# Performance work log

Hardware: AMD Instinct MI355X
Metric: run time of the kernel (lower is better)

## Reference

```python
import jax, jax.numpy as jnp
import numpy as np

T, B, DX, DH, DZ, K = 128, 256, 64, 512, 128, 16


def _lin(x, W, b):
    return x @ W.T + b


def _forget_mult(F, Z, h0):
    # C[t] = F[t]*Z[t] + (1-F[t])*C[t-1], C[-1] = h0; shapes (T,B,H)
    def step(c, fz):
        f, z = fz
        c = f * z + (1.0 - f) * c
        return c, c
    _, C = jax.lax.scan(step, h0, (F, Z))
    return C


def _qrnn_layer(X, W, b, h0):
    # window=1, output_gate=True, zoneout=0 (eval)
    Y = _lin(X, W, b)                      # (T,B,3H)
    Z, F, O = jnp.split(Y, 3, axis=-1)
    C = _forget_mult(jax.nn.sigmoid(F), jnp.tanh(Z), h0)
    return jax.nn.sigmoid(O) * C           # H


def _planar_flow(z, u, w, b):
    # z: (B,T,Dz); u,w: (K,Dz); b: (K,). Returns z_K and summed log-det.
    def m(x):
        return jax.nn.softplus(x) - 1.0
    def step(carry, p):
        z, sldj = carry
        uk, wk, bk = p
        udw = jnp.dot(uk, wk)
        w_hat = wk / jnp.linalg.norm(wk)
        u_hat = (m(udw) - udw) * w_hat + uk
        t = jnp.tanh(z @ wk + bk)          # (B,T)
        z = z + u_hat * t[..., None]
        psi_u = (1.0 - t * t) * jnp.dot(wk, u_hat)
        sldj = sldj - jnp.log(jnp.abs(psi_u + 1.0) + 1e-8)
        return (z, sldj), None
    sldj0 = jnp.zeros(z.shape[:-1], z.dtype)
    (zK, sldj), _ = jax.lax.scan(step, (z, sldj0), (u, w, b))
    return zK, sldj


def _forward(x, y, eps, hs_W, hs_b, q_W, q_b, enc_phi_W, enc_phi_b,
             enc_mean_W, enc_mean_b, enc_std_W, enc_std_b,
             prior_phi_W, prior_phi_b, prior_mean_W, prior_mean_b,
             prior_std_W, prior_std_b, dec_phi_W1, dec_phi_b1,
             dec_phi_W2, dec_phi_b2, dec_mean_W, dec_mean_b,
             dec_std_W, dec_std_b, pnf_u, pnf_w, pnf_b):
    Bsz = x.shape[1]
    Dh = hs_W.shape[0] // 3
    h0 = jnp.zeros((Bsz, Dh), x.dtype)
    # hidden-state QRNN over x
    h = _qrnn_layer(x, hs_W, hs_b, h0)                 # (T,B,Dh)
    # inference QRNN over reversed [y, h]
    rev_in = jnp.concatenate([jnp.flip(y, 0), jnp.flip(h, 0)], axis=-1)
    a = _qrnn_layer(rev_in, q_W, q_b, h0)              # (T,B,Dh)
    rev_a = jnp.swapaxes(jnp.flip(a, 0), 0, 1)         # (B,T,Dh)
    # encoder
    e = jax.nn.relu(_lin(rev_a, enc_phi_W[0], enc_phi_b[0]))
    e = jax.nn.relu(_lin(e, enc_phi_W[1], enc_phi_b[1]))
    enc_mean = jax.nn.sigmoid(_lin(e, enc_mean_W, enc_mean_b))   # (B,T,Dz)
    enc_std = jax.nn.softplus(_lin(e, enc_std_W, enc_std_b))
    z0 = enc_mean + enc_std * eps
    z_k, sldj = _planar_flow(z0, pnf_u, pnf_w, pnf_b)
    # prior
    hp = jnp.swapaxes(h, 0, 1)                          # (B,T,Dh)
    p = jax.nn.relu(_lin(hp, prior_phi_W[0], prior_phi_b[0]))
    p = jax.nn.relu(_lin(p, prior_phi_W[1], prior_phi_b[1]))
    prior_mean = jax.nn.sigmoid(_lin(p, prior_mean_W, prior_mean_b))
    prior_std = jax.nn.softplus(_lin(p, prior_std_W, prior_std_b))
    # decoder
    d = jax.nn.relu(_lin(jnp.concatenate([z_k, hp], axis=-1), dec_phi_W1, dec_phi_b1))
    d = jax.nn.relu(_lin(d, dec_phi_W2, dec_phi_b2))
    dec_mean = jax.nn.sigmoid(_lin(d, dec_mean_W, dec_mean_b))   # (B,T,Dx)
    dec_std = jax.nn.softplus(_lin(d, dec_std_W, dec_std_b))
    return dec_mean, dec_std, enc_mean, enc_std, prior_mean, prior_std, z_k, sldj


def setup_inputs() -> dict:
    key = jax.random.key(0)
    ks = jax.random.split(key, 20)
    def w(i, shape, scale=0.05):
        return (jax.random.normal(ks[i], shape) * scale).astype(jnp.float32)
    return {
        "x": w(0, (T, B, DX), 1.0),
        "y": w(1, (T, B, DX), 1.0),
        "eps": w(2, (B, T, DZ), 1.0),
        "hs_W": w(3, (3 * DH, DX)), "hs_b": jnp.zeros((3 * DH,), jnp.float32),
        "q_W": w(4, (3 * DH, DX + DH)), "q_b": jnp.zeros((3 * DH,), jnp.float32),
        "enc_phi_W": w(5, (2, DH, DH)), "enc_phi_b": jnp.zeros((2, DH), jnp.float32),
        "enc_mean_W": w(6, (DZ, DH)), "enc_mean_b": jnp.zeros((DZ,), jnp.float32),
        "enc_std_W": w(7, (DZ, DH)), "enc_std_b": jnp.zeros((DZ,), jnp.float32),
        "prior_phi_W": w(8, (2, DH, DH)), "prior_phi_b": jnp.zeros((2, DH), jnp.float32),
        "prior_mean_W": w(9, (DZ, DH)), "prior_mean_b": jnp.zeros((DZ,), jnp.float32),
        "prior_std_W": w(10, (DZ, DH)), "prior_std_b": jnp.zeros((DZ,), jnp.float32),
        "dec_phi_W1": w(11, (DH, DH + DZ)), "dec_phi_b1": jnp.zeros((DH,), jnp.float32),
        "dec_phi_W2": w(12, (DH, DH)), "dec_phi_b2": jnp.zeros((DH,), jnp.float32),
        "dec_mean_W": w(13, (DX, DH)), "dec_mean_b": jnp.zeros((DX,), jnp.float32),
        "dec_std_W": w(14, (DX, DH)), "dec_std_b": jnp.zeros((DX,), jnp.float32),
        "pnf_u": w(15, (K, DZ), 0.01), "pnf_w": w(16, (K, DZ), 0.01), "pnf_b": w(17, (K,), 0.01),
    }


def reference(x, y, eps, hs_W, hs_b, q_W, q_b, enc_phi_W, enc_phi_b,
              enc_mean_W, enc_mean_b, enc_std_W, enc_std_b,
              prior_phi_W, prior_phi_b, prior_mean_W, prior_mean_b,
              prior_std_W, prior_std_b, dec_phi_W1, dec_phi_b1,
              dec_phi_W2, dec_phi_b2, dec_mean_W, dec_mean_b,
              dec_std_W, dec_std_b, pnf_u, pnf_w, pnf_b):
    return _forward(x, y, eps, hs_W, hs_b, q_W, q_b, enc_phi_W, enc_phi_b,
                    enc_mean_W, enc_mean_b, enc_std_W, enc_std_b,
                    prior_phi_W, prior_phi_b, prior_mean_W, prior_mean_b,
                    prior_std_W, prior_std_b, dec_phi_W1, dec_phi_b1,
                    dec_phi_W2, dec_phi_b2, dec_mean_W, dec_mean_b,
                    dec_std_W, dec_std_b, pnf_u, pnf_w, pnf_b)
```

## Files before the change

kernel.cpp:

```cpp
#include <hip/hip_runtime.h>
#include <cstddef>
#include <cstdint>

#define DEVI __device__ __forceinline__

namespace {

typedef _Float16 f16;
typedef _Float16 half4 __attribute__((ext_vector_type(4)));
typedef _Float16 half8 __attribute__((ext_vector_type(8)));
typedef _Float16 f16x2 __attribute__((ext_vector_type(2)));
typedef float floatx16 __attribute__((ext_vector_type(16)));

typedef const __attribute__((address_space(1))) void gvoid;
typedef __attribute__((address_space(3))) void lvoid;
#define GLL(gp, lp) __builtin_amdgcn_global_load_lds((gvoid*)(gp), (lvoid*)(lp), 16, 0, 0)

constexpr float kLog2e = 1.4426950408889634f;
constexpr float kLn2   = 0.6931471805599453f;
DEVI float fexp2_(float x) { return __builtin_amdgcn_exp2f(x); }
DEVI float frcp_(float x)  { return __builtin_amdgcn_rcpf(x); }
DEVI float flog2_(float x) { return __builtin_amdgcn_logf(x); }
DEVI float fsig_(float v)  { return frcp_(1.f + fexp2_(-kLog2e * v)); }
DEVI float ftanh_(float v) { return 1.f - 2.f * frcp_(1.f + fexp2_(2.f * kLog2e * v)); }
DEVI float fsoftplus_(float v) {
  return fmaxf(v, 0.f) + kLn2 * flog2_(1.f + fexp2_(-kLog2e * fabsf(v)));
}

struct CvtTab { const float* s[14]; f16* d[14]; int n4[14]; };

__global__ __launch_bounds__(256)
void cvt_k(CvtTab tab) {
  const int e = blockIdx.y;
  const int n4 = tab.n4[e];
  const float4* s = (const float4*)tab.s[e];
  f16* d = tab.d[e];
  for (int i = blockIdx.x * 256 + threadIdx.x; i < n4; i += gridDim.x * 256) {
    const float4 v = s[i];
    half4 o = {(f16)v.x, (f16)v.y, (f16)v.z, (f16)v.w};
    *(half4*)(d + (size_t)i * 4) = o;
  }
}

template <int AM, int OM>
__global__ __launch_bounds__(512, 2)
void gemm16_k(const f16* __restrict__ A0, const f16* __restrict__ A1,
              const f16* __restrict__ W0, const f16* __restrict__ W1,
              const float* __restrict__ bias, const float* __restrict__ bias2,
              float* __restrict__ C, float* __restrict__ C2,
              f16* __restrict__ Ch, int N, int K, int lda, int ntx) {
  __shared__ __align__(16) char lds[131072];
  const int tid = threadIdx.x;
  const int l = tid & 63, w = tid >> 6;
  const int nwg = gridDim.x;
  int bid = blockIdx.x;
  bid = (bid & 7) * (nwg >> 3) + (bid >> 3);
  const int m0 = (bid / ntx) * 256;
  const int n0 = (bid % ntx) * 256;
  const int Nh = N >> 1;

  const f16* pa[4]; const f16* pa2[4]; const f16* pb[4];
#pragma unroll
  for (int r = 0; r < 4; ++r) {
    const int s = r * 512 + tid;
    const int row = s >> 3, c = s & 7;
    const int kc8 = (c ^ (row & 7)) * 8;
    const int m = m0 + row;
    if constexpr (AM == 0) {
      pa[r] = A0 + (size_t)m * lda + kc8;
      pa2[r] = nullptr;
    } else if constexpr (AM == 1) {
      const int t = m >> 8, b = m & 255;
      pa[r]  = A0 + (size_t)((127 - t) * 256 + b) * 64 + kc8;
      pa2[r] = A1 + (size_t)((b << 7) | (127 - t)) * 512 + kc8;
    } else {
      pa[r]  = A0 + (size_t)m * 128 + kc8;
      pa2[r] = A1 + (size_t)m * 512 + kc8;
    }
    int n = n0 + row;
    if constexpr (OM == 2) n = n < N ? n : N - 1;
    if constexpr (OM == 2) {
      pb[r] = (n < Nh ? W0 + (size_t)n * K : W1 + (size_t)(n - Nh) * K) + kc8;
    } else {
      pb[r] = W0 + (size_t)n * K + kc8;
    }
  }

  const int wr = w >> 2, wc = w & 3;
  int offA[4][4], offB[2][4];
#pragma unroll
  for (int mi = 0; mi < 4; ++mi) {
    const int row = wr * 128 + mi * 32 + (l & 31);
#pragma unroll
    for (int s16 = 0; s16 < 4; ++s16) {
      const int c = (s16 * 2 + (l >> 5)) ^ (row & 7);
      offA[mi][s16] = row * 128 + c * 16;
    }
  }
#pragma unroll
  for (int nj = 0; nj < 2; ++nj) {
    const int row = wc * 64 + nj * 32 + (l & 31);
#pragma unroll
    for (int s16 = 0; s16 < 4; ++s16) {
      const int c = (s16 * 2 + (l >> 5)) ^ (row & 7);
      offB[nj][s16] = row * 128 + c * 16;
    }
  }

  float bv[2];
#pragma unroll
  for (int nj = 0; nj < 2; ++nj) {
    int gcol = n0 + wc * 64 + nj * 32 + (l & 31);
    if constexpr (OM == 2) {
      const int gi = gcol < N ? gcol : N - 1;
      bv[nj] = (gi >= Nh) ? bias2[gi - Nh] : bias[gi];
    } else {
      bv[nj] = bias[gcol];
    }
  }
  asm volatile("" : "+v"(bv[0]), "+v"(bv[1]));
  asm volatile("s_waitcnt vmcnt(0)" ::: "memory");

  auto stage = [&](int st, int buf) {
    char* dA = lds + buf * 65536;
    char* dB = dA + 32768;
#pragma unroll
    for (int r = 0; r < 4; ++r) {
      const f16* ga;
      if constexpr (AM == 0)      ga = pa[r] + st * 64;
      else if constexpr (AM == 1) ga = (st == 0) ? pa[r] : (pa2[r] + (st - 1) * 64);
      else                        ga = (st < 2) ? (pa[r] + st * 64) : (pa2[r] + (st - 2) * 64);
      GLL(ga, dA + (r * 512 + w * 64) * 16);
      GLL(pb[r] + st * 64, dB + (r * 512 + w * 64) * 16);
    }
  };

  floatx16 acc[4][2] = {};
  const int nsteps = K >> 6;
  stage(0, 0);
  for (int st = 0; st < nsteps; ++st) {
    const int cur = st & 1;
    if (st + 1 < nsteps) {
      stage(st + 1, cur ^ 1);
      asm volatile("s_waitcnt vmcnt(8)" ::: "memory");
    } else {
      asm volatile("s_waitcnt vmcnt(0)" ::: "memory");
    }
    __builtin_amdgcn_s_barrier();
    __builtin_amdgcn_sched_barrier(0);
    const char* cA = lds + cur * 65536;
    const char* cB = cA + 32768;
#pragma unroll
    for (int s16 = 0; s16 < 4; ++s16) {
      half8 a0 = *(const half8*)(cA + offA[0][s16]);
      half8 a1 = *(const half8*)(cA + offA[1][s16]);
      half8 a2 = *(const half8*)(cA + offA[2][s16]);
      half8 a3 = *(const half8*)(cA + offA[3][s16]);
      half8 b0 = *(const half8*)(cB + offB[0][s16]);
      half8 b1 = *(const half8*)(cB + offB[1][s16]);
      acc[0][0] = __builtin_amdgcn_mfma_f32_32x32x16_f16(a0, b0, acc[0][0], 0, 0, 0);
      acc[0][1] = __builtin_amdgcn_mfma_f32_32x32x16_f16(a0, b1, acc[0][1], 0, 0, 0);
      acc[1][0] = __builtin_amdgcn_mfma_f32_32x32x16_f16(a1, b0, acc[1][0], 0, 0, 0);
      acc[1][1] = __builtin_amdgcn_mfma_f32_32x32x16_f16(a1, b1, acc[1][1], 0, 0, 0);
      acc[2][0] = __builtin_amdgcn_mfma_f32_32x32x16_f16(a2, b0, acc[2][0], 0, 0, 0);
      acc[2][1] = __builtin_amdgcn_mfma_f32_32x32x16_f16(a2, b1, acc[2][1], 0, 0, 0);
      acc[3][0] = __builtin_amdgcn_mfma_f32_32x32x16_f16(a3, b0, acc[3][0], 0, 0, 0);
      acc[3][1] = __builtin_amdgcn_mfma_f32_32x32x16_f16(a3, b1, acc[3][1], 0, 0, 0);
    }
    __builtin_amdgcn_sched_barrier(0);
    asm volatile("s_waitcnt lgkmcnt(0)" ::: "memory");
    __builtin_amdgcn_s_barrier();
  }

  const int col_l = l & 31;
  const int hi4 = (l >> 5) * 4;
#pragma unroll
  for (int nj = 0; nj < 2; ++nj) {
    const int gcol = n0 + wc * 64 + nj * 32 + col_l;
    if constexpr (OM == 2) {
      if (gcol < N) {
        const bool second = gcol >= Nh;
        float* cp = second ? C2 : C;
        const int cl = second ? gcol - Nh : gcol;
#pragma unroll
        for (int mi = 0; mi < 4; ++mi) {
#pragma unroll
          for (int reg = 0; reg < 16; ++reg) {
            const int rl = (reg & 3) + 8 * (reg >> 2) + hi4;
            const int grow = m0 + wr * 128 + mi * 32 + rl;
            const float v = acc[mi][nj][reg] + bv[nj];
            cp[(size_t)grow * Nh + cl] = second ? fsoftplus_(v) : fsig_(v);
          }
        }
      }
    } else {
#pragma unroll
      for (int mi = 0; mi < 4; ++mi) {
#pragma unroll
        for (int reg = 0; reg < 16; ++reg) {
          const int rl = (reg & 3) + 8 * (reg >> 2) + hi4;
          const int grow = m0 + wr * 128 + mi * 32 + rl;
          const float v = acc[mi][nj][reg] + bv[nj];
          float rr;
          if constexpr (OM == 0) rr = (gcol < 512) ? ftanh_(v) : fsig_(v);
          else                   rr = fmaxf(v, 0.f);
          Ch[(size_t)grow * N + gcol] = (f16)rr;
        }
      }
    }
  }
}

template <int MODE>
__global__ __launch_bounds__(256)
void scan_k(const f16* __restrict__ Y, f16* __restrict__ H1) {
  const int idx = blockIdx.x * 256 + threadIdx.x;
  const int b = idx >> 8;
  const int h0 = (idx & 255) * 2;
  float c0 = 0.f, c1 = 0.f;
  for (int t = 0; t < 128; ++t) {
    const f16* p = Y + (size_t)(t * 256 + b) * 1536 + h0;
    const f16x2 zv = *(const f16x2*)(p);
    const f16x2 fv = *(const f16x2*)(p + 512);
    const f16x2 ov = *(const f16x2*)(p + 1024);
    const float f0 = (float)fv[0], f1 = (float)fv[1];
    c0 = f0 * (float)zv[0] + (1.f - f0) * c0;
    c1 = f1 * (float)zv[1] + (1.f - f1) * c1;
    f16x2 hv = {(f16)((float)ov[0] * c0), (f16)((float)ov[1] * c1)};
    const int tt = (MODE == 0) ? t : (127 - t);
    *(f16x2*)(H1 + (size_t)((b << 7) | tt) * 512 + h0) = hv;
  }
}

__global__ __launch_bounds__(256)
void z0_k(const float* __restrict__ mean, const float* __restrict__ sd,
          const float* __restrict__ eps, float* __restrict__ z) {
  const int i = blockIdx.x * 256 + threadIdx.x;
  const float4 m = ((const float4*)mean)[i];
  const float4 s = ((const float4*)sd)[i];
  const float4 e = ((const float4*)eps)[i];
  ((float4*)z)[i] = make_float4(m.x + s.x * e.x, m.y + s.y * e.y,
                                m.z + s.z * e.z, m.w + s.w * e.w);
}

__global__ __launch_bounds__(64)
void flow_pre_k(const float* __restrict__ u, const float* __restrict__ w,
                float* __restrict__ uhat, float* __restrict__ wu) {
  const int k = blockIdx.x, l = threadIdx.x;
  const float w0 = w[k * 128 + l], w1 = w[k * 128 + 64 + l];
  const float u0 = u[k * 128 + l], u1 = u[k * 128 + 64 + l];
  float nrm = w0 * w0 + w1 * w1;
  float udw = u0 * w0 + u1 * w1;
#pragma unroll
  for (int o = 32; o; o >>= 1) { nrm += __shfl_xor(nrm, o); udw += __shfl_xor(udw, o); }
  const float inv = 1.f / sqrtf(nrm);
  const float coef = (fsoftplus_(udw) - 1.f) - udw;
  const float uh0 = coef * (w0 * inv) + u0;
  const float uh1 = coef * (w1 * inv) + u1;
  uhat[k * 128 + l] = uh0;
  uhat[k * 128 + 64 + l] = uh1;
  float dwu = w0 * uh0 + w1 * uh1;
#pragma unroll
  for (int o = 32; o; o >>= 1) dwu += __shfl_xor(dwu, o);
  if (l == 0) wu[k] = dwu;
}

__global__ __launch_bounds__(256)
void flow_k(float* __restrict__ z, const float* __restrict__ w,
            const float* __restrict__ b, const float* __restrict__ uhat,
            const float* __restrict__ wu, float* __restrict__ sldj,
            f16* __restrict__ zh) {
  const int row = blockIdx.x * 4 + (threadIdx.x >> 6);
  const int l = threadIdx.x & 63;
  float* zp = z + (size_t)row * 128;
  float z0 = zp[l], z1 = zp[64 + l];
  float sl = 0.f;
#pragma unroll
  for (int k = 0; k < 16; ++k) {
    const float w0 = w[k * 128 + l], w1 = w[k * 128 + 64 + l];
    float s = z0 * w0 + z1 * w1;
#pragma unroll
    for (int o = 32; o; o >>= 1) s += __shfl_xor(s, o);
    const float t = ftanh_(s + b[k]);
    z0 += uhat[k * 128 + l] * t;
    z1 += uhat[k * 128 + 64 + l] * t;
    const float psi = (1.f - t * t) * wu[k];
    sl -= kLn2 * flog2_(fabsf(psi + 1.f) + 1e-8f);
  }
  zp[l] = z0;
  zp[64 + l] = z1;
  zh[(size_t)row * 128 + l] = (f16)z0;
  zh[(size_t)row * 128 + 64 + l] = (f16)z1;
  if (l == 0) sldj[row] = sl;
}

}

extern "C" void kernel_launch(void* const* d_in, const int* in_sizes, int n_in,
                              void* d_out, int out_size, void* d_ws, size_t ws_size,
                              hipStream_t stream) {
  const float* x           = (const float*)d_in[0];
  const float* y           = (const float*)d_in[1];
  const float* eps         = (const float*)d_in[2];
  const float* hs_b        = (const float*)d_in[4];
  const float* q_b         = (const float*)d_in[6];
  const float* enc_phi_b   = (const float*)d_in[8];
  const float* enc_mean_b  = (const float*)d_in[10];
  const float* enc_std_b   = (const float*)d_in[12];
  const float* prior_phi_b = (const float*)d_in[14];
  const float* prior_mean_b= (const float*)d_in[16];
  const float* prior_std_b = (const float*)d_in[18];
  const float* dec_b1      = (const float*)d_in[20];
  const float* dec_b2      = (const float*)d_in[22];
  const float* dec_mean_b  = (const float*)d_in[24];
  const float* dec_std_b   = (const float*)d_in[26];
  const float* pnf_u       = (const float*)d_in[27];
  const float* pnf_w       = (const float*)d_in[28];
  const float* pnf_b       = (const float*)d_in[29];

  float* out = (float*)d_out;
  float* dec_mean  = out;
  float* dec_std   = out + 2097152;
  float* enc_mean  = out + 4194304;
  float* enc_std   = out + 8388608;
  float* prior_mean= out + 12582912;
  float* prior_std = out + 16777216;
  float* zk        = out + 20971520;
  float* sldj      = out + 25165824;

  char* ws = (char*)d_ws;
  f16* Ybuf  = (f16*)(ws + 0);
  f16* e1    = (f16*)(ws + 0);
  f16* e2    = (f16*)(ws + 33554432);
  f16* arev  = (f16*)(ws + 100663296);
  f16* h_bt  = (f16*)(ws + 134217728);
  f16* zk_h  = (f16*)(ws + 167772160);
  f16* xh    = (f16*)(ws + 176160768);
  f16* yh    = (f16*)(ws + 180355072);
  f16* wbuf  = (f16*)(ws + 184549376);
  float* uhat= (float*)(ws + 190447616);
  float* wu  = (float*)(ws + 190455808);

  f16* w_hs   = wbuf + 0;
  f16* w_q    = wbuf + 98304;
  f16* w_ephi = wbuf + 983040;
  f16* w_emean= wbuf + 1507328;
  f16* w_estd = wbuf + 1572864;
  f16* w_pphi = wbuf + 1638400;
  f16* w_pmean= wbuf + 2162688;
  f16* w_pstd = wbuf + 2228224;
  f16* w_d1   = wbuf + 2293760;
  f16* w_d2   = wbuf + 2621440;
  f16* w_dmean= wbuf + 2883584;
  f16* w_dstd = wbuf + 2916352;

  CvtTab tab;
  const float* srcs[14] = {x, y, (const float*)d_in[3], (const float*)d_in[5],
                           (const float*)d_in[7], (const float*)d_in[9],
                           (const float*)d_in[11], (const float*)d_in[13],
                           (const float*)d_in[15], (const float*)d_in[17],
                           (const float*)d_in[19], (const float*)d_in[21],
                           (const float*)d_in[23], (const float*)d_in[25]};
  f16* dsts[14] = {xh, yh, w_hs, w_q, w_ephi, w_emean, w_estd, w_pphi,
                   w_pmean, w_pstd, w_d1, w_d2, w_dmean, w_dstd};
  const int ns[14] = {2097152, 2097152, 98304, 884736, 524288, 65536, 65536,
                      524288, 65536, 65536, 327680, 262144, 32768, 32768};
  for (int i = 0; i < 14; ++i) { tab.s[i] = srcs[i]; tab.d[i] = dsts[i]; tab.n4[i] = ns[i] >> 2; }
  cvt_k<<<dim3(128, 14), 256, 0, stream>>>(tab);

  const dim3 blk(512);

  gemm16_k<0, 0><<<768, blk, 0, stream>>>(xh, nullptr, w_hs, nullptr,
      hs_b, nullptr, nullptr, nullptr, Ybuf, 1536, 64, 64, 6);
  scan_k<0><<<256, 256, 0, stream>>>(Ybuf, h_bt);

  gemm16_k<1, 0><<<768, blk, 0, stream>>>(yh, h_bt, w_q, nullptr,
      q_b, nullptr, nullptr, nullptr, Ybuf, 1536, 576, 0, 6);
  scan_k<1><<<256, 256, 0, stream>>>(Ybuf, arev);

  gemm16_k<0, 1><<<256, blk, 0, stream>>>(arev, nullptr, w_ephi, nullptr,
      enc_phi_b, nullptr, nullptr, nullptr, e1, 512, 512, 512, 2);
  gemm16_k<0, 1><<<256, blk, 0, stream>>>(e1, nullptr, w_ephi + 262144, nullptr,
      enc_phi_b + 512, nullptr, nullptr, nullptr, e2, 512, 512, 512, 2);
  gemm16_k<0, 2><<<128, blk, 0, stream>>>(e2, nullptr, w_emean, w_estd,
      enc_mean_b, enc_std_b, enc_mean, enc_std, nullptr, 256, 512, 512, 1);
  z0_k<<<4096, 256, 0, stream>>>(enc_mean, enc_std, eps, zk);
  flow_pre_k<<<16, 64, 0, stream>>>(pnf_u, pnf_w, uhat, wu);
  flow_k<<<8192, 256, 0, stream>>>(zk, pnf_w, pnf_b, uhat, wu, sldj, zk_h);

  gemm16_k<0, 1><<<256, blk, 0, stream>>>(h_bt, nullptr, w_pphi, nullptr,
      prior_phi_b, nullptr, nullptr, nullptr, e1, 512, 512, 512, 2);
  gemm16_k<0, 1><<<256, blk, 0, stream>>>(e1, nullptr, w_pphi + 262144, nullptr,
      prior_phi_b + 512, nullptr, nullptr, nullptr, e2, 512, 512, 512, 2);
  gemm16_k<0, 2><<<128, blk, 0, stream>>>(e2, nullptr, w_pmean, w_pstd,
      prior_mean_b, prior_std_b, prior_mean, prior_std, nullptr, 256, 512, 512, 1);

  gemm16_k<2, 1><<<256, blk, 0, stream>>>(zk_h, h_bt, w_d1, nullptr,
      dec_b1, nullptr, nullptr, nullptr, e1, 512, 640, 0, 2);
  gemm16_k<0, 1><<<256, blk, 0, stream>>>(e1, nullptr, w_d2, nullptr,
      dec_b2, nullptr, nullptr, nullptr, e2, 512, 512, 512, 2);
  gemm16_k<0, 2><<<128, blk, 0, stream>>>(e2, nullptr, w_dmean, w_dstd,
      dec_mean_b, dec_std_b, dec_mean, dec_std, nullptr, 128, 512, 512, 1);
}
```

Before: 649.3 us.

## Switch GEMM to 16x16 MFMA with interleaved chunked staging; prefetch scan loads

The GEMM main loop now uses 16x16x32 MFMA tiles (8x4 per wave) and splits the next-stage global-to-LDS copy into four chunks interleaved with compute phases. It adds barriers and s_setprio around each MFMA burst so load issue overlaps matrix work, in place of issuing all loads up front. The scan kernel software-prefetches the next timestep's z/f/o values to hide global load latency in the serial recurrence. The extra barriers per step and a full vmcnt(0) wait at the end of each step may cost some of the intended overlap.

```diff
diff --git a/kernel.cpp b/kernel.cpp
--- a/kernel.cpp
+++ b/kernel.cpp
@@ -10,7 +10,7 @@
 typedef _Float16 half4 __attribute__((ext_vector_type(4)));
 typedef _Float16 half8 __attribute__((ext_vector_type(8)));
 typedef _Float16 f16x2 __attribute__((ext_vector_type(2)));
-typedef float floatx16 __attribute__((ext_vector_type(16)));
+typedef float floatx4 __attribute__((ext_vector_type(4)));
 
 typedef const __attribute__((address_space(1))) void gvoid;
 typedef __attribute__((address_space(3))) void lvoid;
@@ -59,7 +59,7 @@
   const int n0 = (bid % ntx) * 256;
   const int Nh = N >> 1;
 
-  const f16* pa[4]; const f16* pa2[4]; const f16* pb[4];
+  const f16 *pa[4], *pa2[4], *pb[4];
 #pragma unroll
   for (int r = 0; r < 4; ++r) {
     const int s = r * 512 + tid;
@@ -87,120 +87,127 @@
   }
 
   const int wr = w >> 2, wc = w & 3;
-  int offA[4][4], offB[2][4];
-#pragma unroll
-  for (int mi = 0; mi < 4; ++mi) {
-    const int row = wr * 128 + mi * 32 + (l & 31);
-#pragma unroll
-    for (int s16 = 0; s16 < 4; ++s16) {
-      const int c = (s16 * 2 + (l >> 5)) ^ (row & 7);
-      offA[mi][s16] = row * 128 + c * 16;
-    }
-  }
-#pragma unroll
-  for (int nj = 0; nj < 2; ++nj) {
-    const int row = wc * 64 + nj * 32 + (l & 31);
-#pragma unroll
-    for (int s16 = 0; s16 < 4; ++s16) {
-      const int c = (s16 * 2 + (l >> 5)) ^ (row & 7);
-      offB[nj][s16] = row * 128 + c * 16;
-    }
-  }
-
-  float bv[2];
-#pragma unroll
-  for (int nj = 0; nj < 2; ++nj) {
-    int gcol = n0 + wc * 64 + nj * 32 + (l & 31);
+  int offA[8][2], offB[4][2];
+#pragma unroll
+  for (int mf = 0; mf < 8; ++mf) {
+    const int row = wr * 128 + mf * 16 + (l & 15);
+#pragma unroll
+    for (int ks = 0; ks < 2; ++ks) {
+      const int c = (ks * 4 + (l >> 4)) ^ (row & 7);
+      offA[mf][ks] = row * 128 + c * 16;
+    }
+  }
+#pragma unroll
+  for (int nf = 0; nf < 4; ++nf) {
+    const int row = wc * 64 + nf * 16 + (l & 15);
+#pragma unroll
+    for (int ks = 0; ks < 2; ++ks) {
+      const int c = (ks * 4 + (l >> 4)) ^ (row & 7);
+      offB[nf][ks] = row * 128 + c * 16;
+    }
+  }
+
+  float bv[4];
+#pragma unroll
+  for (int nf = 0; nf < 4; ++nf) {
+    int gcol = n0 + wc * 64 + nf * 16 + (l & 15);
     if constexpr (OM == 2) {
       const int gi = gcol < N ? gcol : N - 1;
-      bv[nj] = (gi >= Nh) ? bias2[gi - Nh] : bias[gi];
+      bv[nf] = (gi >= Nh) ? bias2[gi - Nh] : bias[gi];
     } else {
-      bv[nj] = bias[gcol];
-    }
-  }
-  asm volatile("" : "+v"(bv[0]), "+v"(bv[1]));
-  asm volatile("s_waitcnt vmcnt(0)" ::: "memory");
-
-  auto stage = [&](int st, int buf) {
+      bv[nf] = bias[gcol];
+    }
+  }
+
+  auto stage_chunk = [&](int st, int buf, int p) {
     char* dA = lds + buf * 65536;
     char* dB = dA + 32768;
 #pragma unroll
-    for (int r = 0; r < 4; ++r) {
-      const f16* ga;
-      if constexpr (AM == 0)      ga = pa[r] + st * 64;
-      else if constexpr (AM == 1) ga = (st == 0) ? pa[r] : (pa2[r] + (st - 1) * 64);
-      else                        ga = (st < 2) ? (pa[r] + st * 64) : (pa2[r] + (st - 2) * 64);
-      GLL(ga, dA + (r * 512 + w * 64) * 16);
-      GLL(pb[r] + st * 64, dB + (r * 512 + w * 64) * 16);
+    for (int q = 0; q < 2; ++q) {
+      const int r = (p & 1) * 2 + q;
+      if (p < 2) {
+        const f16* ga;
+        if constexpr (AM == 0)      ga = pa[r] + st * 64;
+        else if constexpr (AM == 1) ga = (st == 0) ? pa[r] : (pa2[r] + (st - 1) * 64);
+        else                        ga = (st < 2) ? (pa[r] + st * 64) : (pa2[r] + (st - 2) * 64);
+        GLL(ga, dA + (r * 512 + w * 64) * 16);
+      } else {
+        GLL(pb[r] + st * 64, dB + (r * 512 + w * 64) * 16);
+      }
     }
   };
 
-  floatx16 acc[4][2] = {};
+  floatx4 acc[8][4] = {};
   const int nsteps = K >> 6;
-  stage(0, 0);
-  for (int st = 0; st < nsteps; ++st) {
-    const int cur = st & 1;
-    if (st + 1 < nsteps) {
-      stage(st + 1, cur ^ 1);
-      asm volatile("s_waitcnt vmcnt(8)" ::: "memory");
-    } else {
-      asm volatile("s_waitcnt vmcnt(0)" ::: "memory");
-    }
+#pragma unroll
+  for (int p = 0; p < 4; ++p) stage_chunk(0, 0, p);
+  asm volatile("s_waitcnt vmcnt(0)" ::: "memory");
+  __builtin_amdgcn_s_barrier();
+
+  for (int t = 0; t < nsteps; ++t) {
+    const int s = t & 1;
+    const char* cA = lds + s * 65536;
+    const char* cB = cA + 32768;
+    const bool more = (t + 1 < nsteps);
+    half8 bfr[4];
+#pragma unroll
+    for (int p = 0; p < 4; ++p) {
+      if (more) stage_chunk(t + 1, s ^ 1, p);
+      constexpr int dummy = 0; (void)dummy;
+      const int ks = p >> 1;
+      if ((p & 1) == 0) {
+        bfr[0] = *(const half8*)(cB + offB[0][ks]);
+        bfr[1] = *(const half8*)(cB + offB[1][ks]);
+        bfr[2] = *(const half8*)(cB + offB[2][ks]);
+        bfr[3] = *(const half8*)(cB + offB[3][ks]);
+      }
+      half8 afr[4];
+#pragma unroll
+      for (int mi = 0; mi < 4; ++mi)
+        afr[mi] = *(const half8*)(cA + offA[(p & 1) * 4 + mi][ks]);
+      __builtin_amdgcn_s_barrier();
+      __builtin_amdgcn_s_setprio(1);
+#pragma unroll
+      for (int mi = 0; mi < 4; ++mi) {
+#pragma unroll
+        for (int nf = 0; nf < 4; ++nf) {
+          acc[(p & 1) * 4 + mi][nf] = __builtin_amdgcn_mfma_f32_16x16x32_f16(
+              afr[mi], bfr[nf], acc[(p & 1) * 4 + mi][nf], 0, 0, 0);
+        }
+      }
+      __builtin_amdgcn_s_setprio(0);
+      __builtin_amdgcn_s_barrier();
+    }
+    asm volatile("s_waitcnt lgkmcnt(0) vmcnt(0)" ::: "memory");
     __builtin_amdgcn_s_barrier();
-    __builtin_amdgcn_sched_barrier(0);
-    const char* cA = lds + cur * 65536;
-    const char* cB = cA + 32768;
-#pragma unroll
-    for (int s16 = 0; s16 < 4; ++s16) {
-      half8 a0 = *(const half8*)(cA + offA[0][s16]);
-      half8 a1 = *(const half8*)(cA + offA[1][s16]);
-      half8 a2 = *(const half8*)(cA + offA[2][s16]);
-      half8 a3 = *(const half8*)(cA + offA[3][s16]);
-      half8 b0 = *(const half8*)(cB + offB[0][s16]);
-      half8 b1 = *(const half8*)(cB + offB[1][s16]);
-      acc[0][0] = __builtin_amdgcn_mfma_f32_32x32x16_f16(a0, b0, acc[0][0], 0, 0, 0);
-      acc[0][1] = __builtin_amdgcn_mfma_f32_32x32x16_f16(a0, b1, acc[0][1], 0, 0, 0);
-      acc[1][0] = __builtin_amdgcn_mfma_f32_32x32x16_f16(a1, b0, acc[1][0], 0, 0, 0);
-      acc[1][1] = __builtin_amdgcn_mfma_f32_32x32x16_f16(a1, b1, acc[1][1], 0, 0, 0);
-      acc[2][0] = __builtin_amdgcn_mfma_f32_32x32x16_f16(a2, b0, acc[2][0], 0, 0, 0);
-      acc[2][1] = __builtin_amdgcn_mfma_f32_32x32x16_f16(a2, b1, acc[2][1], 0, 0, 0);
-      acc[3][0] = __builtin_amdgcn_mfma_f32_32x32x16_f16(a3, b0, acc[3][0], 0, 0, 0);
-      acc[3][1] = __builtin_amdgcn_mfma_f32_32x32x16_f16(a3, b1, acc[3][1], 0, 0, 0);
-    }
-    __builtin_amdgcn_sched_barrier(0);
-    asm volatile("s_waitcnt lgkmcnt(0)" ::: "memory");
-    __builtin_amdgcn_s_barrier();
-  }
-
-  const int col_l = l & 31;
-  const int hi4 = (l >> 5) * 4;
-#pragma unroll
-  for (int nj = 0; nj < 2; ++nj) {
-    const int gcol = n0 + wc * 64 + nj * 32 + col_l;
+  }
+
+  const int r0 = (l >> 4) * 4;
+#pragma unroll
+  for (int nf = 0; nf < 4; ++nf) {
+    const int gcol = n0 + wc * 64 + nf * 16 + (l & 15);
     if constexpr (OM == 2) {
       if (gcol < N) {
         const bool second = gcol >= Nh;
         float* cp = second ? C2 : C;
         const int cl = second ? gcol - Nh : gcol;
 #pragma unroll
-        for (int mi = 0; mi < 4; ++mi) {
-#pragma unroll
-          for (int reg = 0; reg < 16; ++reg) {
-            const int rl = (reg & 3) + 8 * (reg >> 2) + hi4;
-            const int grow = m0 + wr * 128 + mi * 32 + rl;
-            const float v = acc[mi][nj][reg] + bv[nj];
+        for (int mf = 0; mf < 8; ++mf) {
+#pragma unroll
+          for (int reg = 0; reg < 4; ++reg) {
+            const int grow = m0 + wr * 128 + mf * 16 + r0 + reg;
+            const float v = acc[mf][nf][reg] + bv[nf];
             cp[(size_t)grow * Nh + cl] = second ? fsoftplus_(v) : fsig_(v);
           }
         }
       }
     } else {
 #pragma unroll
-      for (int mi = 0; mi < 4; ++mi) {
-#pragma unroll
-        for (int reg = 0; reg < 16; ++reg) {
-          const int rl = (reg & 3) + 8 * (reg >> 2) + hi4;
-          const int grow = m0 + wr * 128 + mi * 32 + rl;
-          const float v = acc[mi][nj][reg] + bv[nj];
+      for (int mf = 0; mf < 8; ++mf) {
+#pragma unroll
+        for (int reg = 0; reg < 4; ++reg) {
+          const int grow = m0 + wr * 128 + mf * 16 + r0 + reg;
+          const float v = acc[mf][nf][reg] + bv[nf];
           float rr;
           if constexpr (OM == 0) rr = (gcol < 512) ? ftanh_(v) : fsig_(v);
           else                   rr = fmaxf(v, 0.f);
@@ -218,17 +225,26 @@
   const int b = idx >> 8;
   const int h0 = (idx & 255) * 2;
   float c0 = 0.f, c1 = 0.f;
+  const f16* pt = Y + (size_t)b * 1536 + h0;
+  f16x2 zv = *(const f16x2*)(pt);
+  f16x2 fv = *(const f16x2*)(pt + 512);
+  f16x2 ov = *(const f16x2*)(pt + 1024);
   for (int t = 0; t < 128; ++t) {
-    const f16* p = Y + (size_t)(t * 256 + b) * 1536 + h0;
-    const f16x2 zv = *(const f16x2*)(p);
-    const f16x2 fv = *(const f16x2*)(p + 512);
-    const f16x2 ov = *(const f16x2*)(p + 1024);
+    const f16* nx = pt + 256 * 1536;
+    f16x2 zn, fn, on;
+    if (t < 127) {
+      zn = *(const f16x2*)(nx);
+      fn = *(const f16x2*)(nx + 512);
+      on = *(const f16x2*)(nx + 1024);
+    }
     const float f0 = (float)fv[0], f1 = (float)fv[1];
     c0 = f0 * (float)zv[0] + (1.f - f0) * c0;
     c1 = f1 * (float)zv[1] + (1.f - f1) * c1;
     f16x2 hv = {(f16)((float)ov[0] * c0), (f16)((float)ov[1] * c1)};
     const int tt = (MODE == 0) ? t : (127 - t);
     *(f16x2*)(H1 + (size_t)((b << 7) | tt) * 512 + h0) = hv;
+    zv = zn; fv = fn; ov = on;
+    pt = nx;
   }
 }
 
```

After: 694.4 us. 6.9% more time.
